# Optimization experiments

Measured on AMD Instinct MI355X. Metric: run time of the kernel, lower is better.

The kernel has to match this reference:

```python
import jax, jax.numpy as jnp
import numpy as np

B, D, H, W = 32, 64, 32, 32   # batch, laten_dim, latent spatial dims
K = 2048                      # codebook_size


def setup_inputs() -> dict:
    key = jax.random.key(0)
    k1, k2 = jax.random.split(key)
    laten = jax.random.normal(k1, (B, D, H, W), dtype=jnp.float32)
    codebook = jax.random.normal(k2, (K, D), dtype=jnp.float32)
    return {"laten": laten, "codebook": codebook}


def reference(laten, codebook):
    # Faithful jax translation of VQVAE.quant_laten.
    b, c, h, w = laten.shape
    # (b, c, h, w) -> (b*h*w, c)
    x = jnp.transpose(laten, (0, 2, 3, 1)).reshape(-1, c)  # (N, D)
    # avoids materializing the (N, K, D) broadcast intermediate.
    x_sq = jnp.sum(x * x, axis=-1, keepdims=True)          # (N, 1)
    e_sq = jnp.sum(codebook * codebook, axis=-1)           # (K,)
    l2_distance = (x_sq - 2.0 * (x @ codebook.T) + e_sq) / c  # (N, K)
    closest_idx_2d = jnp.argmin(l2_distance, axis=-1).reshape(b, h, w)
    # gather + permute(0, 3, 1, 2)
    quant_laten = jnp.transpose(codebook[closest_idx_2d], (0, 3, 1, 2))
    return closest_idx_2d, quant_laten
```

## Files before the change

### kernel.cpp

```cpp
#include <hip/hip_runtime.h>

#define N_PIX 32768
#define DIM   64
#define KCODE 2048

typedef __attribute__((ext_vector_type(8))) short bf16x8;
typedef __attribute__((ext_vector_type(4))) float f32x4;

__device__ inline unsigned short f2bf(float v) {
    unsigned int u = __float_as_uint(v);
    return (unsigned short)((u + 0x7FFFu + ((u >> 16) & 1u)) >> 16);
}
__device__ inline float bf2f(unsigned short b) {
    return __uint_as_float(((unsigned int)b) << 16);
}

__global__ __launch_bounds__(256)
void convert_b_kernel(const float* __restrict__ cb, unsigned short* __restrict__ Bg,
                      float* __restrict__ esq) {
    const int t   = blockIdx.x * 256 + threadIdx.x;
    const int n   = t >> 4;
    const int sub = t & 15;
    const int ntile = n >> 4, ni = n & 15;

    const float4 v = *(const float4*)(cb + (size_t)n * DIM + sub * 4);

    unsigned int h01, h23, m01, m23, l01, l23;
    {
        unsigned short h, m, l;
        float r1;
        h = f2bf(v.x); r1 = v.x - bf2f(h); m = f2bf(r1); l = f2bf(r1 - bf2f(m));
        h01 = h;       m01 = m;       l01 = l;
        h = f2bf(v.y); r1 = v.y - bf2f(h); m = f2bf(r1); l = f2bf(r1 - bf2f(m));
        h01 |= (unsigned int)h << 16; m01 |= (unsigned int)m << 16; l01 |= (unsigned int)l << 16;
        h = f2bf(v.z); r1 = v.z - bf2f(h); m = f2bf(r1); l = f2bf(r1 - bf2f(m));
        h23 = h;       m23 = m;       l23 = l;
        h = f2bf(v.w); r1 = v.w - bf2f(h); m = f2bf(r1); l = f2bf(r1 - bf2f(m));
        h23 |= (unsigned int)h << 16; m23 |= (unsigned int)m << 16; l23 |= (unsigned int)l << 16;
    }

    float s = (v.x * v.x + v.y * v.y) + (v.z * v.z + v.w * v.w);
#pragma unroll
    for (int mk = 1; mk < 16; mk <<= 1) s += __shfl_xor(s, mk, 16);
    if (sub == 0) esq[n] = s;

    char* outb = (char*)Bg;
    const size_t u = ((((size_t)ntile) * 8 + (sub >> 1)) << 8) + ni * 16 + (sub & 1) * 8;
    uint2 hw2 = {h01, h23}, mw2 = {m01, m23}, lw2 = {l01, l23};
    *(uint2*)(outb + u)          = hw2;
    *(uint2*)(outb + 262144 + u) = mw2;
    *(uint2*)(outb + 524288 + u) = lw2;
}

#define DO_PASS(APL, BPL)                                                    \
    _Pragma("unroll") for (int ks = 0; ks < 2; ++ks)                         \
    _Pragma("unroll") for (int mt = 0; mt < 2; ++mt)                         \
        acc[mt] = __builtin_amdgcn_mfma_f32_16x16x32_bf16(                   \
            af[APL][mt][ks], bfr[BPL][ks], acc[mt], 0, 0, 0);

#define LOAD_BFR(PL)                                                         \
    _Pragma("unroll") for (int ks = 0; ks < 2; ++ks)                         \
        bfr[PL][ks] = *(const bf16x8*)(rb + (PL) * 8192 + ks * 1024 + lane * 16);

__device__ __forceinline__ void stage_unit(const char* BgB, char* ringBase,
                                           int u, int it, int slotOff, int lane) {
    const int pl = u >> 3, rem = u & 7, g = rem >> 1, ks = rem & 1;
    const char* gsrc = BgB + (size_t)pl * 262144 + (size_t)(g * 32 + it) * 2048
                     + ks * 1024 + lane * 16;
    char* ldst = ringBase + slotOff + pl * 8192 + g * 2048 + ks * 1024;
    __builtin_amdgcn_global_load_lds(
        (const __attribute__((address_space(1))) void*)gsrc,
        (__attribute__((address_space(3))) void*)ldst, 16, 0, 0);
}

#define ITER(J, DOSTAGE, VM)                                                 \
  {                                                                          \
    if (DOSTAGE) {                                                           \
      const int so2 = (((J) + 2) % 3) * 24576;                               \
      stage_unit(BgB, ring, wave,      (J) + 2, so2, lane);                  \
      stage_unit(BgB, ring, wave + 8,  (J) + 2, so2, lane);                  \
      stage_unit(BgB, ring, wave + 16, (J) + 2, so2, lane);                  \
    }                                                                        \
    asm volatile("s_waitcnt vmcnt(" #VM ")" ::: "memory");                   \
    __builtin_amdgcn_s_barrier();                                            \
    asm volatile("" ::: "memory");                                           \
    const char* rb = ring + (((J) % 3) * 24576) + wn * 2048;                 \
    bf16x8 bfr[3][2];                                                        \
    LOAD_BFR(2)                                                              \
    LOAD_BFR(0)                                                              \
    LOAD_BFR(1)                                                              \
    f32x4 acc[2];                                                            \
    acc[0] = f32x4{0.f, 0.f, 0.f, 0.f};                                      \
    acc[1] = f32x4{0.f, 0.f, 0.f, 0.f};                                      \
    __builtin_amdgcn_s_setprio(1);                                           \
    DO_PASS(0, 2)                                                            \
    DO_PASS(2, 0)                                                            \
    DO_PASS(1, 1)                                                            \
    DO_PASS(0, 1)                                                            \
    DO_PASS(1, 0)                                                            \
    DO_PASS(0, 0)                                                            \
    __builtin_amdgcn_s_setprio(0);                                           \
    const int n = wn * 512 + (J) * 16 + col;                                 \
    const float e = esqS[n];                                                 \
    _Pragma("unroll") for (int mt = 0; mt < 2; ++mt)                         \
    _Pragma("unroll") for (int r = 0; r < 4; ++r) {                          \
      float d = fmaf(-2.f, acc[mt][r], e);                                   \
      if (d < best[mt][r]) { best[mt][r] = d; bidx[mt][r] = n; }             \
    }                                                                        \
    asm volatile("s_waitcnt lgkmcnt(0)" ::: "memory");                       \
    __builtin_amdgcn_s_barrier();                                            \
    asm volatile("" ::: "memory");                                           \
  }

__global__ __launch_bounds__(512, 4)
void dist_fused_kernel(const float* __restrict__ laten,
                       const unsigned short* __restrict__ Bg,
                       const float* __restrict__ esq,
                       const float* __restrict__ cb,
                       float* __restrict__ out0, float* __restrict__ out1) {
    __shared__ __align__(16) char ring[73728];
    __shared__ float esqS[2048];

    const int tid  = threadIdx.x;
    const int lane = tid & 63;
    const int wave = tid >> 6;
    const int wm   = wave & 1;
    const int wn   = wave >> 1;
    const int quad = lane >> 4, col = lane & 15;
    const int bx = blockIdx.x;
    const int bb = bx >> 4, hw0 = (bx & 15) * 64;

    const char* BgB = (const char*)Bg;

    {
        const int p = tid & 63, dg = tid >> 6;
        const float* srcA = laten + (size_t)bb * 65536 + (size_t)dg * 8192 + hw0 + p;
        const int mt = p >> 4, mi = p & 15;
        alignas(16) unsigned short hv[8], mv[8], lv[8];
#pragma unroll
        for (int j = 0; j < 8; ++j) {
            float v = srcA[(size_t)j << 10];
            unsigned short h = f2bf(v);
            float r1 = v - bf2f(h);
            unsigned short m = f2bf(r1);
            unsigned short l = f2bf(r1 - bf2f(m));
            hv[j] = h; mv[j] = m; lv[j] = l;
        }
        int u = ((mt * 8 + dg) << 8) + mi * 16;
        *(uint4*)(ring + u)         = *(uint4*)hv;
        *(uint4*)(ring + 8192 + u)  = *(uint4*)mv;
        *(uint4*)(ring + 16384 + u) = *(uint4*)lv;
    }
    *(float4*)(esqS + tid * 4) = *(const float4*)(esq + tid * 4);
    __syncthreads();

    bf16x8 af[3][2][2];
#pragma unroll
    for (int pl = 0; pl < 3; ++pl)
#pragma unroll
        for (int mt = 0; mt < 2; ++mt)
#pragma unroll
            for (int ks = 0; ks < 2; ++ks)
                af[pl][mt][ks] = *(const bf16x8*)(ring + pl * 8192
                    + (((wm * 2 + mt) * 8 + ks * 4 + quad) << 8) + col * 16);
    __syncthreads();

    stage_unit(BgB, ring, wave,      0, 0, lane);
    stage_unit(BgB, ring, wave + 8,  0, 0, lane);
    stage_unit(BgB, ring, wave + 16, 0, 0, lane);
    stage_unit(BgB, ring, wave,      1, 24576, lane);
    stage_unit(BgB, ring, wave + 8,  1, 24576, lane);
    stage_unit(BgB, ring, wave + 16, 1, 24576, lane);

    float best[2][4];
    int   bidx[2][4];
#pragma unroll
    for (int mt = 0; mt < 2; ++mt)
#pragma unroll
        for (int r = 0; r < 4; ++r) { best[mt][r] = 3.4e38f; bidx[mt][r] = 0; }

    for (int it = 0; it < 30; ++it) ITER(it, true, 6)
    ITER(30, false, 3)
    ITER(31, false, 0)

    float* redD = (float*)ring;
    int*   redI = (int*)(ring + 1024);
    int*   idxF = (int*)(ring + 2048);
#pragma unroll
    for (int mt = 0; mt < 2; ++mt)
#pragma unroll
        for (int r = 0; r < 4; ++r) {
            float d = best[mt][r];
            int   i = bidx[mt][r];
#pragma unroll
            for (int m = 1; m < 16; m <<= 1) {
                float od = __shfl_xor(d, m, 16);
                int   oi = __shfl_xor(i, m, 16);
                if (od < d || (od == d && oi < i)) { d = od; i = oi; }
            }
            if (col == 0) {
                int row = wm * 32 + mt * 16 + quad * 4 + r;
                redD[row * 4 + wn] = d;
                redI[row * 4 + wn] = i;
            }
        }
    __syncthreads();

    if (tid < 64) {
        float bd = redD[tid * 4]; int bi = redI[tid * 4];
#pragma unroll
        for (int w = 1; w < 4; ++w) {
            float d = redD[tid * 4 + w]; int i = redI[tid * 4 + w];
            if (d < bd || (d == bd && i < bi)) { bd = d; bi = i; }
        }
        out0[bx * 64 + tid] = (float)bi;
        idxF[tid] = bi;
    }
    __syncthreads();

    const int p = tid & 63, dg = tid >> 6;
    const int idx = idxF[p];
    const float4* srcr = (const float4*)(cb + ((size_t)idx << 6) + dg * 8);
    float* o = out1 + (size_t)bb * 65536 + (size_t)dg * 8192 + hw0 + p;
    float4 v0 = srcr[0], v1 = srcr[1];
    o[(size_t)0 << 10] = v0.x; o[(size_t)1 << 10] = v0.y;
    o[(size_t)2 << 10] = v0.z; o[(size_t)3 << 10] = v0.w;
    o[(size_t)4 << 10] = v1.x; o[(size_t)5 << 10] = v1.y;
    o[(size_t)6 << 10] = v1.z; o[(size_t)7 << 10] = v1.w;
}

extern "C" void kernel_launch(void* const* d_in, const int* in_sizes, int n_in,
                              void* d_out, int out_size, void* d_ws, size_t ws_size,
                              hipStream_t stream) {
    const float* laten = (const float*)d_in[0];
    const float* cb    = (const float*)d_in[1];

    float* out0 = (float*)d_out;
    float* out1 = (float*)d_out + N_PIX;

    float* esq = (float*)d_ws;
    unsigned short* Bg = (unsigned short*)(esq + 2048);

    convert_b_kernel<<<128, 256, 0, stream>>>(cb, Bg, esq);

    dist_fused_kernel<<<512, 512, 0, stream>>>(laten, Bg, esq, cb, out0, out1);
}
```

Measured before the change: 106.2 us.

## Use 4 waves each covering all 64 rows, double-buffer B fragments in registers

After: 107.8 us. About the same (+1.6%).

```diff
diff --git a/kernel.cpp b/kernel.cpp
--- a/kernel.cpp
+++ b/kernel.cpp
@@ -52,15 +52,16 @@
     *(uint2*)(outb + 524288 + u) = lw2;
 }
 
-#define DO_PASS(APL, BPL)                                                    \
+#define DO_PASS(APL, BPL, B)                                                 \
     _Pragma("unroll") for (int ks = 0; ks < 2; ++ks)                         \
-    _Pragma("unroll") for (int mt = 0; mt < 2; ++mt)                         \
+    _Pragma("unroll") for (int mt = 0; mt < 4; ++mt)                         \
         acc[mt] = __builtin_amdgcn_mfma_f32_16x16x32_bf16(                   \
-            af[APL][mt][ks], bfr[BPL][ks], acc[mt], 0, 0, 0);
-
-#define LOAD_BFR(PL)                                                         \
+            af[APL][mt][ks], B[BPL][ks], acc[mt], 0, 0, 0);
+
+#define LOAD_B(DST, RB)                                                      \
+    _Pragma("unroll") for (int pl = 0; pl < 3; ++pl)                         \
     _Pragma("unroll") for (int ks = 0; ks < 2; ++ks)                         \
-        bfr[PL][ks] = *(const bf16x8*)(rb + (PL) * 8192 + ks * 1024 + lane * 16);
+        DST[pl][ks] = *(const bf16x8*)((RB) + pl * 8192 + ks * 1024 + lane * 16);
 
 __device__ __forceinline__ void stage_unit(const char* BgB, char* ringBase,
                                            int u, int it, int slotOff, int lane) {
@@ -73,59 +74,59 @@
         (__attribute__((address_space(3))) void*)ldst, 16, 0, 0);
 }
 
-#define ITER(J, DOSTAGE, VM)                                                 \
+#define STAGE6(T, SO)                                                        \
+    stage_unit(BgB, ring, 0 * 8 + wn * 2 + 0, (T), (SO), lane);              \
+    stage_unit(BgB, ring, 0 * 8 + wn * 2 + 1, (T), (SO), lane);              \
+    stage_unit(BgB, ring, 1 * 8 + wn * 2 + 0, (T), (SO), lane);              \
+    stage_unit(BgB, ring, 1 * 8 + wn * 2 + 1, (T), (SO), lane);              \
+    stage_unit(BgB, ring, 2 * 8 + wn * 2 + 0, (T), (SO), lane);              \
+    stage_unit(BgB, ring, 2 * 8 + wn * 2 + 1, (T), (SO), lane);
+
+#define ITER(J, BCUR, BNXT, DOSTAGE, DOREAD, VM)                             \
   {                                                                          \
-    if (DOSTAGE) {                                                           \
-      const int so2 = (((J) + 2) % 3) * 24576;                               \
-      stage_unit(BgB, ring, wave,      (J) + 2, so2, lane);                  \
-      stage_unit(BgB, ring, wave + 8,  (J) + 2, so2, lane);                  \
-      stage_unit(BgB, ring, wave + 16, (J) + 2, so2, lane);                  \
+    if (DOSTAGE) { STAGE6((J) + 2, ((J) & 1) * 24576) }                      \
+    asm volatile("s_waitcnt vmcnt(" #VM ")" ::: "memory");                   \
+    if (DOREAD) {                                                            \
+      const char* rb = ring + (((J) + 1) & 1) * 24576 + wn * 2048;           \
+      LOAD_B(BNXT, rb)                                                       \
     }                                                                        \
-    asm volatile("s_waitcnt vmcnt(" #VM ")" ::: "memory");                   \
+    f32x4 acc[4];                                                            \
+    acc[0] = f32x4{0.f, 0.f, 0.f, 0.f};                                      \
+    acc[1] = f32x4{0.f, 0.f, 0.f, 0.f};                                      \
+    acc[2] = f32x4{0.f, 0.f, 0.f, 0.f};                                      \
+    acc[3] = f32x4{0.f, 0.f, 0.f, 0.f};                                      \
+    __builtin_amdgcn_s_setprio(1);                                           \
+    DO_PASS(0, 2, BCUR)                                                      \
+    DO_PASS(2, 0, BCUR)                                                      \
+    DO_PASS(1, 1, BCUR)                                                      \
+    DO_PASS(0, 1, BCUR)                                                      \
+    DO_PASS(1, 0, BCUR)                                                      \
+    DO_PASS(0, 0, BCUR)                                                      \
+    __builtin_amdgcn_s_setprio(0);                                           \
+    asm volatile("s_waitcnt lgkmcnt(0)" ::: "memory");                       \
     __builtin_amdgcn_s_barrier();                                            \
     asm volatile("" ::: "memory");                                           \
-    const char* rb = ring + (((J) % 3) * 24576) + wn * 2048;                 \
-    bf16x8 bfr[3][2];                                                        \
-    LOAD_BFR(2)                                                              \
-    LOAD_BFR(0)                                                              \
-    LOAD_BFR(1)                                                              \
-    f32x4 acc[2];                                                            \
-    acc[0] = f32x4{0.f, 0.f, 0.f, 0.f};                                      \
-    acc[1] = f32x4{0.f, 0.f, 0.f, 0.f};                                      \
-    __builtin_amdgcn_s_setprio(1);                                           \
-    DO_PASS(0, 2)                                                            \
-    DO_PASS(2, 0)                                                            \
-    DO_PASS(1, 1)                                                            \
-    DO_PASS(0, 1)                                                            \
-    DO_PASS(1, 0)                                                            \
-    DO_PASS(0, 0)                                                            \
-    __builtin_amdgcn_s_setprio(0);                                           \
     const int n = wn * 512 + (J) * 16 + col;                                 \
     const float e = esqS[n];                                                 \
-    _Pragma("unroll") for (int mt = 0; mt < 2; ++mt)                         \
+    _Pragma("unroll") for (int mt = 0; mt < 4; ++mt)                         \
     _Pragma("unroll") for (int r = 0; r < 4; ++r) {                          \
       float d = fmaf(-2.f, acc[mt][r], e);                                   \
       if (d < best[mt][r]) { best[mt][r] = d; bidx[mt][r] = n; }             \
     }                                                                        \
-    asm volatile("s_waitcnt lgkmcnt(0)" ::: "memory");                       \
-    __builtin_amdgcn_s_barrier();                                            \
-    asm volatile("" ::: "memory");                                           \
   }
 
-__global__ __launch_bounds__(512, 4)
+__global__ __launch_bounds__(256, 2)
 void dist_fused_kernel(const float* __restrict__ laten,
                        const unsigned short* __restrict__ Bg,
                        const float* __restrict__ esq,
                        const float* __restrict__ cb,
                        float* __restrict__ out0, float* __restrict__ out1) {
-    __shared__ __align__(16) char ring[73728];
+    __shared__ __align__(16) char ring[49152];
     __shared__ float esqS[2048];
 
     const int tid  = threadIdx.x;
     const int lane = tid & 63;
-    const int wave = tid >> 6;
-    const int wm   = wave & 1;
-    const int wn   = wave >> 1;
+    const int wn   = tid >> 6;
     const int quad = lane >> 4, col = lane & 15;
     const int bx = blockIdx.x;
     const int bb = bx >> 4, hw0 = (bx & 15) * 64;
@@ -133,61 +134,71 @@
     const char* BgB = (const char*)Bg;
 
     {
-        const int p = tid & 63, dg = tid >> 6;
-        const float* srcA = laten + (size_t)bb * 65536 + (size_t)dg * 8192 + hw0 + p;
+        const int p = tid & 63, dgp = tid >> 6;
         const int mt = p >> 4, mi = p & 15;
-        alignas(16) unsigned short hv[8], mv[8], lv[8];
-#pragma unroll
-        for (int j = 0; j < 8; ++j) {
-            float v = srcA[(size_t)j << 10];
-            unsigned short h = f2bf(v);
-            float r1 = v - bf2f(h);
-            unsigned short m = f2bf(r1);
-            unsigned short l = f2bf(r1 - bf2f(m));
-            hv[j] = h; mv[j] = m; lv[j] = l;
+#pragma unroll
+        for (int dd = 0; dd < 2; ++dd) {
+            const int dg = dgp * 2 + dd;
+            const float* srcA = laten + (size_t)bb * 65536 + (size_t)dg * 8192 + hw0 + p;
+            alignas(16) unsigned short hv[8], mv[8], lv[8];
+#pragma unroll
+            for (int j = 0; j < 8; ++j) {
+                float v = srcA[(size_t)j << 10];
+                unsigned short h = f2bf(v);
+                float r1 = v - bf2f(h);
+                unsigned short m = f2bf(r1);
+                unsigned short l = f2bf(r1 - bf2f(m));
+                hv[j] = h; mv[j] = m; lv[j] = l;
+            }
+            int u = ((mt * 8 + dg) << 8) + mi * 16;
+            *(uint4*)(ring + u)         = *(uint4*)hv;
+            *(uint4*)(ring + 8192 + u)  = *(uint4*)mv;
+            *(uint4*)(ring + 16384 + u) = *(uint4*)lv;
         }
-        int u = ((mt * 8 + dg) << 8) + mi * 16;
-        *(uint4*)(ring + u)         = *(uint4*)hv;
-        *(uint4*)(ring + 8192 + u)  = *(uint4*)mv;
-        *(uint4*)(ring + 16384 + u) = *(uint4*)lv;
-    }
-    *(float4*)(esqS + tid * 4) = *(const float4*)(esq + tid * 4);
-    __syncthreads();
-
-    bf16x8 af[3][2][2];
+    }
+    *(float4*)(esqS + tid * 8)     = *(const float4*)(esq + tid * 8);
+    *(float4*)(esqS + tid * 8 + 4) = *(const float4*)(esq + tid * 8 + 4);
+    __syncthreads();
+
+    bf16x8 af[3][4][2];
 #pragma unroll
     for (int pl = 0; pl < 3; ++pl)
 #pragma unroll
-        for (int mt = 0; mt < 2; ++mt)
+        for (int mt = 0; mt < 4; ++mt)
 #pragma unroll
             for (int ks = 0; ks < 2; ++ks)
                 af[pl][mt][ks] = *(const bf16x8*)(ring + pl * 8192
-                    + (((wm * 2 + mt) * 8 + ks * 4 + quad) << 8) + col * 16);
-    __syncthreads();
-
-    stage_unit(BgB, ring, wave,      0, 0, lane);
-    stage_unit(BgB, ring, wave + 8,  0, 0, lane);
-    stage_unit(BgB, ring, wave + 16, 0, 0, lane);
-    stage_unit(BgB, ring, wave,      1, 24576, lane);
-    stage_unit(BgB, ring, wave + 8,  1, 24576, lane);
-    stage_unit(BgB, ring, wave + 16, 1, 24576, lane);
-
-    float best[2][4];
-    int   bidx[2][4];
-#pragma unroll
-    for (int mt = 0; mt < 2; ++mt)
+                    + ((mt * 8 + ks * 4 + quad) << 8) + col * 16);
+    __syncthreads();
+
+    STAGE6(0, 0)
+    STAGE6(1, 24576)
+    asm volatile("s_waitcnt vmcnt(6)" ::: "memory");
+    bf16x8 bfrA[3][2], bfrB[3][2];
+    LOAD_B(bfrA, ring + wn * 2048)
+    asm volatile("s_waitcnt lgkmcnt(0)" ::: "memory");
+    __builtin_amdgcn_s_barrier();
+    asm volatile("" ::: "memory");
+
+    float best[4][4];
+    int   bidx[4][4];
+#pragma unroll
+    for (int mt = 0; mt < 4; ++mt)
 #pragma unroll
         for (int r = 0; r < 4; ++r) { best[mt][r] = 3.4e38f; bidx[mt][r] = 0; }
 
-    for (int it = 0; it < 30; ++it) ITER(it, true, 6)
-    ITER(30, false, 3)
-    ITER(31, false, 0)
+    for (int j = 0; j < 30; j += 2) {
+        ITER(j,     bfrA, bfrB, true, true, 6)
+        ITER(j + 1, bfrB, bfrA, true, true, 6)
+    }
+    ITER(30, bfrA, bfrB, false, true, 0)
+    ITER(31, bfrB, bfrA, false, false, 0)
 
     float* redD = (float*)ring;
     int*   redI = (int*)(ring + 1024);
     int*   idxF = (int*)(ring + 2048);
 #pragma unroll
-    for (int mt = 0; mt < 2; ++mt)
+    for (int mt = 0; mt < 4; ++mt)
 #pragma unroll
         for (int r = 0; r < 4; ++r) {
             float d = best[mt][r];
@@ -199,7 +210,7 @@
                 if (od < d || (od == d && oi < i)) { d = od; i = oi; }
             }
             if (col == 0) {
-                int row = wm * 32 + mt * 16 + quad * 4 + r;
+                int row = mt * 16 + quad * 4 + r;
                 redD[row * 4 + wn] = d;
                 redI[row * 4 + wn] = i;
             }
@@ -218,15 +229,19 @@
     }
     __syncthreads();
 
-    const int p = tid & 63, dg = tid >> 6;
+    const int p = tid & 63, dgp = tid >> 6;
     const int idx = idxF[p];
-    const float4* srcr = (const float4*)(cb + ((size_t)idx << 6) + dg * 8);
-    float* o = out1 + (size_t)bb * 65536 + (size_t)dg * 8192 + hw0 + p;
-    float4 v0 = srcr[0], v1 = srcr[1];
-    o[(size_t)0 << 10] = v0.x; o[(size_t)1 << 10] = v0.y;
-    o[(size_t)2 << 10] = v0.z; o[(size_t)3 << 10] = v0.w;
-    o[(size_t)4 << 10] = v1.x; o[(size_t)5 << 10] = v1.y;
-    o[(size_t)6 << 10] = v1.z; o[(size_t)7 << 10] = v1.w;
+    const float4* srcr = (const float4*)(cb + ((size_t)idx << 6) + dgp * 16);
+    float* o = out1 + (size_t)bb * 65536 + (size_t)dgp * 16384 + hw0 + p;
+    float4 v0 = srcr[0], v1 = srcr[1], v2 = srcr[2], v3 = srcr[3];
+    o[(size_t)0  << 10] = v0.x; o[(size_t)1  << 10] = v0.y;
+    o[(size_t)2  << 10] = v0.z; o[(size_t)3  << 10] = v0.w;
+    o[(size_t)4  << 10] = v1.x; o[(size_t)5  << 10] = v1.y;
+    o[(size_t)6  << 10] = v1.z; o[(size_t)7  << 10] = v1.w;
+    o[(size_t)8  << 10] = v2.x; o[(size_t)9  << 10] = v2.y;
+    o[(size_t)10 << 10] = v2.z; o[(size_t)11 << 10] = v2.w;
+    o[(size_t)12 << 10] = v3.x; o[(size_t)13 << 10] = v3.y;
+    o[(size_t)14 << 10] = v3.z; o[(size_t)15 << 10] = v3.w;
 }
 
 extern "C" void kernel_launch(void* const* d_in, const int* in_sizes, int n_in,
@@ -243,5 +258,5 @@
 
     convert_b_kernel<<<128, 256, 0, stream>>>(cb, Bg, esq);
 
-    dist_fused_kernel<<<512, 512, 0, stream>>>(laten, Bg, esq, cb, out0, out1);
-}
+    dist_fused_kernel<<<512, 256, 0, stream>>>(laten, Bg, esq, cb, out0, out1);
+}
```

## Load codebook fragments directly from global into registers, drop LDS ring and barriers

Applied to the files above, without the earlier changes.

Result: slower. 136.7 us (+28.8%).

```diff
diff --git a/kernel.cpp b/kernel.cpp
--- a/kernel.cpp
+++ b/kernel.cpp
@@ -52,54 +52,37 @@
     *(uint2*)(outb + 524288 + u) = lw2;
 }
 
-#define DO_PASS(APL, BPL)                                                    \
+#define DO_PASS(APL, BPL, B)                                                 \
     _Pragma("unroll") for (int ks = 0; ks < 2; ++ks)                         \
     _Pragma("unroll") for (int mt = 0; mt < 2; ++mt)                         \
         acc[mt] = __builtin_amdgcn_mfma_f32_16x16x32_bf16(                   \
-            af[APL][mt][ks], bfr[BPL][ks], acc[mt], 0, 0, 0);
-
-#define LOAD_BFR(PL)                                                         \
-    _Pragma("unroll") for (int ks = 0; ks < 2; ++ks)                         \
-        bfr[PL][ks] = *(const bf16x8*)(rb + (PL) * 8192 + ks * 1024 + lane * 16);
-
-__device__ __forceinline__ void stage_unit(const char* BgB, char* ringBase,
-                                           int u, int it, int slotOff, int lane) {
-    const int pl = u >> 3, rem = u & 7, g = rem >> 1, ks = rem & 1;
-    const char* gsrc = BgB + (size_t)pl * 262144 + (size_t)(g * 32 + it) * 2048
-                     + ks * 1024 + lane * 16;
-    char* ldst = ringBase + slotOff + pl * 8192 + g * 2048 + ks * 1024;
-    __builtin_amdgcn_global_load_lds(
-        (const __attribute__((address_space(1))) void*)gsrc,
-        (__attribute__((address_space(3))) void*)ldst, 16, 0, 0);
-}
-
-#define ITER(J, DOSTAGE, VM)                                                 \
+            af[APL][mt][ks], B[BPL][ks], acc[mt], 0, 0, 0);
+
+#define GLOAD_B(DST, IT)                                                     \
   {                                                                          \
-    if (DOSTAGE) {                                                           \
-      const int so2 = (((J) + 2) % 3) * 24576;                               \
-      stage_unit(BgB, ring, wave,      (J) + 2, so2, lane);                  \
-      stage_unit(BgB, ring, wave + 8,  (J) + 2, so2, lane);                  \
-      stage_unit(BgB, ring, wave + 16, (J) + 2, so2, lane);                  \
-    }                                                                        \
-    asm volatile("s_waitcnt vmcnt(" #VM ")" ::: "memory");                   \
-    __builtin_amdgcn_s_barrier();                                            \
-    asm volatile("" ::: "memory");                                           \
-    const char* rb = ring + (((J) % 3) * 24576) + wn * 2048;                 \
-    bf16x8 bfr[3][2];                                                        \
-    LOAD_BFR(2)                                                              \
-    LOAD_BFR(0)                                                              \
-    LOAD_BFR(1)                                                              \
+    const char* gb = bp0 + (size_t)(IT) * 2048;                              \
+    DST[2][0] = *(const bf16x8*)(gb + 524288);                               \
+    DST[2][1] = *(const bf16x8*)(gb + 524288 + 1024);                        \
+    DST[0][0] = *(const bf16x8*)(gb);                                        \
+    DST[0][1] = *(const bf16x8*)(gb + 1024);                                 \
+    DST[1][0] = *(const bf16x8*)(gb + 262144);                               \
+    DST[1][1] = *(const bf16x8*)(gb + 262144 + 1024);                        \
+  }
+
+#define ITER(J, BCUR, PRE)                                                   \
+  {                                                                          \
     f32x4 acc[2];                                                            \
     acc[0] = f32x4{0.f, 0.f, 0.f, 0.f};                                      \
     acc[1] = f32x4{0.f, 0.f, 0.f, 0.f};                                      \
     __builtin_amdgcn_s_setprio(1);                                           \
-    DO_PASS(0, 2)                                                            \
-    DO_PASS(2, 0)                                                            \
-    DO_PASS(1, 1)                                                            \
-    DO_PASS(0, 1)                                                            \
-    DO_PASS(1, 0)                                                            \
-    DO_PASS(0, 0)                                                            \
+    DO_PASS(0, 2, BCUR)                                                      \
+    DO_PASS(2, 0, BCUR)                                                      \
+    DO_PASS(1, 1, BCUR)                                                      \
+    DO_PASS(0, 1, BCUR)                                                      \
+    DO_PASS(1, 0, BCUR)                                                      \
+    DO_PASS(0, 0, BCUR)                                                      \
     __builtin_amdgcn_s_setprio(0);                                           \
+    if (PRE) GLOAD_B(BCUR, (J) + 2)                                          \
     const int n = wn * 512 + (J) * 16 + col;                                 \
     const float e = esqS[n];                                                 \
     _Pragma("unroll") for (int mt = 0; mt < 2; ++mt)                         \
@@ -107,9 +90,6 @@
       float d = fmaf(-2.f, acc[mt][r], e);                                   \
       if (d < best[mt][r]) { best[mt][r] = d; bidx[mt][r] = n; }             \
     }                                                                        \
-    asm volatile("s_waitcnt lgkmcnt(0)" ::: "memory");                       \
-    __builtin_amdgcn_s_barrier();                                            \
-    asm volatile("" ::: "memory");                                           \
   }
 
 __global__ __launch_bounds__(512, 4)
@@ -118,7 +98,7 @@
                        const float* __restrict__ esq,
                        const float* __restrict__ cb,
                        float* __restrict__ out0, float* __restrict__ out1) {
-    __shared__ __align__(16) char ring[73728];
+    __shared__ __align__(16) char ring[24576];
     __shared__ float esqS[2048];
 
     const int tid  = threadIdx.x;
@@ -131,6 +111,7 @@
     const int bb = bx >> 4, hw0 = (bx & 15) * 64;
 
     const char* BgB = (const char*)Bg;
+    const char* bp0 = BgB + (size_t)(wn * 32) * 2048 + lane * 16;
 
     {
         const int p = tid & 63, dg = tid >> 6;
@@ -165,12 +146,9 @@
                     + (((wm * 2 + mt) * 8 + ks * 4 + quad) << 8) + col * 16);
     __syncthreads();
 
-    stage_unit(BgB, ring, wave,      0, 0, lane);
-    stage_unit(BgB, ring, wave + 8,  0, 0, lane);
-    stage_unit(BgB, ring, wave + 16, 0, 0, lane);
-    stage_unit(BgB, ring, wave,      1, 24576, lane);
-    stage_unit(BgB, ring, wave + 8,  1, 24576, lane);
-    stage_unit(BgB, ring, wave + 16, 1, 24576, lane);
+    bf16x8 bfrA[3][2], bfrB[3][2];
+    GLOAD_B(bfrA, 0)
+    GLOAD_B(bfrB, 1)
 
     float best[2][4];
     int   bidx[2][4];
@@ -179,9 +157,10 @@
 #pragma unroll
         for (int r = 0; r < 4; ++r) { best[mt][r] = 3.4e38f; bidx[mt][r] = 0; }
 
-    for (int it = 0; it < 30; ++it) ITER(it, true, 6)
-    ITER(30, false, 3)
-    ITER(31, false, 0)
+    for (int j = 0; j < 32; j += 2) {
+        ITER(j,     bfrA, (j) + 2 < 32)
+        ITER(j + 1, bfrB, (j) + 3 < 32)
+    }
 
     float* redD = (float*)ring;
     int*   redI = (int*)(ring + 1024);
```
